# Kernel tuning notes

Measured on AMD Instinct MI355X. Metric: run time of the kernel, lower is better.

## Reference

```python
import jax, jax.numpy as jnp
import numpy as np

HE, WE, L = 361, 720, 37   # ERA5 source grid (0.5 deg) and pressure levels
HM, WM, K = 180, 360, 32   # model grid (1 deg) and model sigma levels
EPS = 1e-8

# ERA5 standard 37 pressure levels in Pa (ascending)
P_LEVELS = [100., 200., 300., 500., 700., 1000., 2000., 3000., 5000., 7000.,
            10000., 12500., 15000., 17500., 20000., 22500., 25000., 30000.,
            35000., 40000., 45000., 50000., 55000., 60000., 65000., 70000.,
            75000., 77500., 80000., 82500., 85000., 87500., 90000., 92500.,
            95000., 97500., 100000.]


def setup_inputs() -> dict:
    key = jax.random.key(0)
    ks = jax.random.split(key, 6)
    u = 10.0 * jax.random.normal(ks[0], (HE, WE, L), jnp.float32)
    v = 10.0 * jax.random.normal(ks[1], (HE, WE, L), jnp.float32)
    w = 0.1 * jax.random.normal(ks[2], (HE, WE, L), jnp.float32)
    T = 250.0 + 30.0 * jax.random.normal(ks[3], (HE, WE, L), jnp.float32)
    q = 0.01 * jax.random.uniform(ks[4], (HE, WE, L), jnp.float32)
    ps = 95000.0 + 5000.0 * jax.random.normal(ks[5], (HE, WE), jnp.float32)
    era5_lat = jnp.linspace(-90.0, 90.0, HE, dtype=jnp.float32)
    era5_lon = jnp.linspace(0.0, 359.5, WE, dtype=jnp.float32)
    model_lat = jnp.linspace(-89.0, 89.0, HM, dtype=jnp.float32)
    model_lon = jnp.linspace(0.25, 359.75, WM, dtype=jnp.float32)
    p_levels = jnp.asarray(P_LEVELS, jnp.float32)
    b_k = ((jnp.arange(K, dtype=jnp.float32) + 0.5) / K)
    a_k = 100.0 * (1.0 - b_k)  # simple hybrid coefficients (Pa)
    return dict(u=u, v=v, w=w, T=T, q=q, ps=ps,
                era5_lat=era5_lat, era5_lon=era5_lon,
                model_lat=model_lat, model_lon=model_lon,
                p_levels=p_levels, a_k=a_k, b_k=b_k)


def _axis_interp(grid, pts):
    """1D linear interp indices/weights with linear extrapolation (fill_value=None)."""
    i = jnp.clip(jnp.searchsorted(grid, pts, side='right') - 1, 0, grid.shape[0] - 2)
    t = (pts - grid[i]) / (grid[i + 1] - grid[i])
    return i, t


def _forward(u, v, w, T, q, ps, era5_lat, era5_lon, model_lat, model_lon,
             p_levels, a_k, b_k):
    # ---- horizontal bilinear interp (RegularGridInterpolator, linear) ----
    stacked = jnp.concatenate([u, v, w, T, q, ps[..., None]], axis=-1)  # [HE,WE,5L+1]
    iy, ty = _axis_interp(era5_lat, model_lat)   # [HM]
    ix, tx = _axis_interp(era5_lon, model_lon)   # [WM]
    r0 = stacked[iy]       # [HM,WE,C]
    r1 = stacked[iy + 1]
    d00, d01 = r0[:, ix], r0[:, ix + 1]          # [HM,WM,C]
    d10, d11 = r1[:, ix], r1[:, ix + 1]
    wy = ty[:, None, None]
    wx = tx[None, :, None]
    hd = (1 - wy) * ((1 - wx) * d00 + wx * d01) + wy * ((1 - wx) * d10 + wx * d11)
    vars_h = hd[..., :5 * L].reshape(HM, WM, 5, L)  # [HM,WM,5,L]
    ps_m = hd[..., -1]                               # [HM,WM]

    # ---- model pressure: p = a_k + b_k * ps ----
    p_model = a_k + b_k * ps_m[..., None]            # [HM,WM,K]

    # ---- vertical log-pressure linear interp with per-pixel valid mask ----
    logp_e = jnp.log(p_levels + EPS)                 # [L]
    logp_m = jnp.log(p_model + EPS)                  # [HM,WM,K]
    nvalid = jnp.searchsorted(p_levels, ps_m, side='right')  # levels with p<=ps
    idx = jnp.searchsorted(logp_e, logp_m, side='right') - 1
    idx = jnp.clip(idx, 0, jnp.maximum(nvalid[..., None] - 2, 0))  # [HM,WM,K]
    x0, x1 = logp_e[idx], logp_e[idx + 1]
    t = (logp_m - x0) / (x1 - x0)                    # linear extrapolation at edges
    g0 = jnp.take_along_axis(vars_h, idx[:, :, None, :], axis=3)        # [HM,WM,5,K]
    g1 = jnp.take_along_axis(vars_h, (idx + 1)[:, :, None, :], axis=3)
    out = g0 + t[:, :, None, :] * (g1 - g0)
    out = jnp.where(nvalid[:, :, None, None] >= 2, out, 0.0)            # <2 valid -> 0

    # ---- unit conversion / clamps ----
    u_o, v_o, w_o = out[:, :, 0], out[:, :, 1], out[:, :, 2]
    T_o = jnp.clip(out[:, :, 3], 150.0, 350.0)
    q_o = jnp.clip(out[:, :, 4], 0.0, 0.05)
    ps_o = jnp.clip(ps_m, 30000.0, 110000.0)
    out3d = jnp.stack([u_o, v_o, w_o, T_o, q_o], axis=-1)  # [HM,WM,K,5]
    return out3d, p_model, ps_o


def reference(u, v, w, T, q, ps, era5_lat, era5_lon, model_lat, model_lon,
              p_levels, a_k, b_k):
    return _forward(u, v, w, T, q, ps, era5_lat, era5_lon,
                    model_lat, model_lon, p_levels, a_k, b_k)
```

## Files before the change

kernel.cpp:

```cpp
#include <hip/hip_runtime.h>
#include <cmath>

#define HE 361
#define WE 720
#define LL 37
#define HM 180
#define WM 360
#define KK 32
#define NPTS (HM * WM)
#define EPSF 1e-8f
#define PTSB 8

#define OFF1 ((size_t)HM * WM * KK * 5)
#define OFF2 (OFF1 + (size_t)HM * WM * KK)

#define WS_IY    0
#define WS_TY    180
#define WS_IX    360
#define WS_TX    720
#define WS_LOGPE 1080

__device__ __forceinline__ int upper_bound_g(const float* a, int n, float v) {
    int lo = 0, hi = n;
    while (lo < hi) {
        int m = (lo + hi) >> 1;
        if (a[m] <= v) lo = m + 1; else hi = m;
    }
    return lo;
}

__global__ void precompute_kernel(const float* __restrict__ era5_lat,
                                  const float* __restrict__ era5_lon,
                                  const float* __restrict__ model_lat,
                                  const float* __restrict__ model_lon,
                                  const float* __restrict__ p_levels,
                                  int* __restrict__ ws_iy, float* __restrict__ ws_ty,
                                  int* __restrict__ ws_ix, float* __restrict__ ws_tx,
                                  float* __restrict__ ws_logpe) {
    int t = blockIdx.x * blockDim.x + threadIdx.x;
    if (t < HM) {
        float v = model_lat[t];
        int i = upper_bound_g(era5_lat, HE, v) - 1;
        if (i < 0) i = 0;
        if (i > HE - 2) i = HE - 2;
        ws_iy[t] = i;
        ws_ty[t] = (v - era5_lat[i]) / (era5_lat[i + 1] - era5_lat[i]);
    } else if (t < HM + WM) {
        int j = t - HM;
        float v = model_lon[j];
        int i = upper_bound_g(era5_lon, WE, v) - 1;
        if (i < 0) i = 0;
        if (i > WE - 2) i = WE - 2;
        ws_ix[j] = i;
        ws_tx[j] = (v - era5_lon[i]) / (era5_lon[i + 1] - era5_lon[i]);
    } else if (t < HM + WM + LL) {
        int k = t - HM - WM;
        ws_logpe[k] = logf(p_levels[k] + EPSF);
    }
}

__global__ void __launch_bounds__(256)
fused_kernel(const float* __restrict__ u, const float* __restrict__ v,
             const float* __restrict__ w, const float* __restrict__ T,
             const float* __restrict__ q, const float* __restrict__ ps,
             const float* __restrict__ p_levels,
             const float* __restrict__ a_k, const float* __restrict__ b_k,
             const int* __restrict__ ws_iy, const float* __restrict__ ws_ty,
             const int* __restrict__ ws_ix, const float* __restrict__ ws_tx,
             const float* __restrict__ ws_logpe,
             float* __restrict__ out) {
    __shared__ float s_h[PTSB][5 * LL];
    __shared__ float s_psm[PTSB];
    __shared__ float s_plev[LL];
    __shared__ float s_logpe[LL];
    __shared__ float s_ak[KK];
    __shared__ float s_bk[KK];

    const int tid = threadIdx.x;
    if (tid < LL) {
        s_plev[tid]  = p_levels[tid];
        s_logpe[tid] = ws_logpe[tid];
    } else if (tid >= 64 && tid < 64 + KK) {
        s_ak[tid - 64] = a_k[tid - 64];
        s_bk[tid - 64] = b_k[tid - 64];
    }

    const int pt_local = tid >> 5;
    const int grp      = tid & 31;
    const int pt = blockIdx.x * PTSB + pt_local;
    const int y  = pt / WM;
    const int x  = pt - y * WM;

    const int   iy = ws_iy[y];
    const float ty = ws_ty[y];
    const int   ix = ws_ix[x];
    const float tx = ws_tx[x];
    const float omty = 1.0f - ty;
    const float omtx = 1.0f - tx;

    const size_t b00 = (size_t)iy * WE + ix;

    if (grp == 0) {
        const float p00 = ps[b00], p01 = ps[b00 + 1];
        const float p10 = ps[b00 + WE], p11 = ps[b00 + WE + 1];
        const float ps_m = omty * (omtx * p00 + tx * p01) + ty * (omtx * p10 + tx * p11);
        s_psm[pt_local] = ps_m;
        out[OFF2 + pt] = fminf(fmaxf(ps_m, 30000.0f), 110000.0f);
    }

    const float* srcs0 = u;
    const float* srcs1 = v;
    const float* srcs2 = w;
    const float* srcs3 = T;
    const float* srcs4 = q;

#pragma unroll
    for (int it = 0; it < 6; it++) {
        const int ch = grp + 32 * it;
        if (ch < 5 * LL) {
            const int var = ch / LL;
            const int l   = ch - var * LL;
            const float* s = (var == 0) ? srcs0 : (var == 1) ? srcs1
                           : (var == 2) ? srcs2 : (var == 3) ? srcs3 : srcs4;
            const size_t c00 = b00 * LL + l;
            const float d00 = s[c00];
            const float d01 = s[c00 + LL];
            const float d10 = s[c00 + (size_t)WE * LL];
            const float d11 = s[c00 + (size_t)WE * LL + LL];
            s_h[pt_local][ch] = omty * (omtx * d00 + tx * d01) +
                                ty   * (omtx * d10 + tx * d11);
        }
    }

    __syncthreads();

    const int k = grp;
    const float ps_m = s_psm[pt_local];

    int nvalid = 0;
#pragma unroll
    for (int l = 0; l < LL; l++) nvalid += (s_plev[l] <= ps_m) ? 1 : 0;
    int maxi = nvalid - 2;
    if (maxi < 0) maxi = 0;

    const float pm = s_ak[k] + s_bk[k] * ps_m;
    out[OFF1 + (size_t)pt * KK + k] = pm;

    const float lpm = logf(pm + EPSF);
    int lo = 0, hi = LL;
    while (lo < hi) {
        int m = (lo + hi) >> 1;
        if (s_logpe[m] <= lpm) lo = m + 1; else hi = m;
    }
    int i = lo - 1;
    if (i < 0) i = 0;
    if (i > maxi) i = maxi;
    const float t = (lpm - s_logpe[i]) / (s_logpe[i + 1] - s_logpe[i]);

    const bool invalid = (nvalid < 2);
    const size_t obase = (size_t)pt * (KK * 5) + k * 5;
#pragma unroll
    for (int var = 0; var < 5; var++) {
        const float g0 = s_h[pt_local][var * LL + i];
        const float g1 = s_h[pt_local][var * LL + i + 1];
        float o = g0 + t * (g1 - g0);
        if (invalid) o = 0.0f;
        if (var == 3) o = fminf(fmaxf(o, 150.0f), 350.0f);
        if (var == 4) o = fminf(fmaxf(o, 0.0f), 0.05f);
        out[obase + var] = o;
    }
}

extern "C" void kernel_launch(void* const* d_in, const int* in_sizes, int n_in,
                              void* d_out, int out_size, void* d_ws, size_t ws_size,
                              hipStream_t stream) {
    const float* u         = (const float*)d_in[0];
    const float* v         = (const float*)d_in[1];
    const float* w         = (const float*)d_in[2];
    const float* T         = (const float*)d_in[3];
    const float* q         = (const float*)d_in[4];
    const float* ps        = (const float*)d_in[5];
    const float* era5_lat  = (const float*)d_in[6];
    const float* era5_lon  = (const float*)d_in[7];
    const float* model_lat = (const float*)d_in[8];
    const float* model_lon = (const float*)d_in[9];
    const float* p_levels  = (const float*)d_in[10];
    const float* a_k       = (const float*)d_in[11];
    const float* b_k       = (const float*)d_in[12];

    float* wsf = (float*)d_ws;
    int*   ws_iy    = (int*)(wsf + WS_IY);
    float* ws_ty    = wsf + WS_TY;
    int*   ws_ix    = (int*)(wsf + WS_IX);
    float* ws_tx    = wsf + WS_TX;
    float* ws_logpe = wsf + WS_LOGPE;

    float* out = (float*)d_out;

    precompute_kernel<<<3, 256, 0, stream>>>(era5_lat, era5_lon, model_lat, model_lon,
                                             p_levels, ws_iy, ws_ty, ws_ix, ws_tx,
                                             ws_logpe);

    const int blocks = NPTS / PTSB;
    fused_kernel<<<blocks, 256, 0, stream>>>(u, v, w, T, q, ps, p_levels, a_k, b_k,
                                             ws_iy, ws_ty, ws_ix, ws_tx, ws_logpe, out);
}
```

Baseline: 231.0 us.

## Stage shared source columns into LDS via global_load_lds and defer horizontal interp

Each block now stages a 2-row by 9-column patch of all five source variables (all 37 levels) into LDS using the asynchronous global_load_lds path, instead of having each point gather its own 4 corners. Horizontal bilinear interpolation is deferred and done per output level only for the two bracketing pressure levels, reading corners from LDS. Adjacent model points share source columns, so the change aims to remove redundant global gathers and register staging. It keeps a global-memory fallback for points whose columns fall outside the staged patch. The cost is a larger LDS footprint and more corner reads per output level, which may reduce occupancy.

```diff
diff --git a/kernel.cpp b/kernel.cpp
--- a/kernel.cpp
+++ b/kernel.cpp
@@ -1,5 +1,6 @@
 #include <hip/hip_runtime.h>
 #include <cmath>
+#include <stdint.h>
 
 #define HE 361
 #define WE 720
@@ -10,6 +11,11 @@
 #define NPTS (HM * WM)
 #define EPSF 1e-8f
 #define PTSB 8
+#define NC 9
+#define NSEG (2 * NC * 5)
+#define TOTF (NSEG * LL)
+#define NIT ((TOTF + 255) / 256)
+#define LDSF (NIT * 256)
 
 #define OFF1 ((size_t)HM * WM * KK * 5)
 #define OFF2 (OFF1 + (size_t)HM * WM * KK)
@@ -69,7 +75,7 @@
              const int* __restrict__ ws_ix, const float* __restrict__ ws_tx,
              const float* __restrict__ ws_logpe,
              float* __restrict__ out) {
-    __shared__ float s_h[PTSB][5 * LL];
+    __shared__ float s_cols[LDSF];
     __shared__ float s_psm[PTSB];
     __shared__ float s_plev[LL];
     __shared__ float s_logpe[LL];
@@ -77,6 +83,35 @@
     __shared__ float s_bk[KK];
 
     const int tid = threadIdx.x;
+    const int pt0 = blockIdx.x * PTSB;
+    const int y   = pt0 / WM;
+    const int x0  = pt0 - y * WM;
+
+    const int   iy    = ws_iy[y];
+    const int   colLo = ws_ix[x0];
+
+    const int wavebase = __builtin_amdgcn_readfirstlane(tid & ~63);
+#pragma unroll
+    for (int it = 0; it < NIT; it++) {
+        int idx = it * 256 + tid;
+        int idc = (idx < TOTF) ? idx : (TOTF - 1);
+        int seg = idc / LL;
+        int l   = idc - seg * LL;
+        int r   = seg / (NC * 5);
+        int rem = seg - r * (NC * 5);
+        int c   = rem / 5;
+        int var = rem - c * 5;
+        int col = colLo + c;
+        if (col > WE - 1) col = WE - 1;
+        const float* sp = (var == 0) ? u : (var == 1) ? v : (var == 2) ? w
+                        : (var == 3) ? T : q;
+        const float* ga = sp + ((size_t)(iy + r) * WE + col) * LL + l;
+        __builtin_amdgcn_global_load_lds(
+            (const __attribute__((address_space(1))) uint32_t*)ga,
+            (__attribute__((address_space(3))) uint32_t*)&s_cols[it * 256 + wavebase],
+            4, 0, 0);
+    }
+
     if (tid < LL) {
         s_plev[tid]  = p_levels[tid];
         s_logpe[tid] = ws_logpe[tid];
@@ -87,20 +122,17 @@
 
     const int pt_local = tid >> 5;
     const int grp      = tid & 31;
-    const int pt = blockIdx.x * PTSB + pt_local;
-    const int y  = pt / WM;
-    const int x  = pt - y * WM;
-
-    const int   iy = ws_iy[y];
+    const int pt = pt0 + pt_local;
+    const int x  = x0 + pt_local;
+
     const float ty = ws_ty[y];
-    const int   ix = ws_ix[x];
     const float tx = ws_tx[x];
+    const int   ixp = ws_ix[x];
     const float omty = 1.0f - ty;
     const float omtx = 1.0f - tx;
 
-    const size_t b00 = (size_t)iy * WE + ix;
-
     if (grp == 0) {
+        const size_t b00 = (size_t)iy * WE + ixp;
         const float p00 = ps[b00], p01 = ps[b00 + 1];
         const float p10 = ps[b00 + WE], p11 = ps[b00 + WE + 1];
         const float ps_m = omty * (omtx * p00 + tx * p01) + ty * (omtx * p10 + tx * p11);
@@ -108,30 +140,6 @@
         out[OFF2 + pt] = fminf(fmaxf(ps_m, 30000.0f), 110000.0f);
     }
 
-    const float* srcs0 = u;
-    const float* srcs1 = v;
-    const float* srcs2 = w;
-    const float* srcs3 = T;
-    const float* srcs4 = q;
-
-#pragma unroll
-    for (int it = 0; it < 6; it++) {
-        const int ch = grp + 32 * it;
-        if (ch < 5 * LL) {
-            const int var = ch / LL;
-            const int l   = ch - var * LL;
-            const float* s = (var == 0) ? srcs0 : (var == 1) ? srcs1
-                           : (var == 2) ? srcs2 : (var == 3) ? srcs3 : srcs4;
-            const size_t c00 = b00 * LL + l;
-            const float d00 = s[c00];
-            const float d01 = s[c00 + LL];
-            const float d10 = s[c00 + (size_t)WE * LL];
-            const float d11 = s[c00 + (size_t)WE * LL + LL];
-            s_h[pt_local][ch] = omty * (omtx * d00 + tx * d01) +
-                                ty   * (omtx * d10 + tx * d11);
-        }
-    }
-
     __syncthreads();
 
     const int k = grp;
@@ -159,15 +167,49 @@
 
     const bool invalid = (nvalid < 2);
     const size_t obase = (size_t)pt * (KK * 5) + k * 5;
-#pragma unroll
-    for (int var = 0; var < 5; var++) {
-        const float g0 = s_h[pt_local][var * LL + i];
-        const float g1 = s_h[pt_local][var * LL + i + 1];
-        float o = g0 + t * (g1 - g0);
-        if (invalid) o = 0.0f;
-        if (var == 3) o = fminf(fmaxf(o, 150.0f), 350.0f);
-        if (var == 4) o = fminf(fmaxf(o, 0.0f), 0.05f);
-        out[obase + var] = o;
+
+    const int cpt = ixp - colLo;
+    if (cpt >= 0 && cpt <= NC - 2) {
+        const int o00 = (cpt * 5) * LL;
+        const int o01 = ((cpt + 1) * 5) * LL;
+        const int o10 = ((NC + cpt) * 5) * LL;
+        const int o11 = ((NC + cpt + 1) * 5) * LL;
+#pragma unroll
+        for (int var = 0; var < 5; var++) {
+            const int vb = var * LL + i;
+            const float a0 = s_cols[o00 + vb],     b0 = s_cols[o01 + vb];
+            const float c0 = s_cols[o10 + vb],     d0 = s_cols[o11 + vb];
+            const float a1 = s_cols[o00 + vb + 1], b1 = s_cols[o01 + vb + 1];
+            const float c1 = s_cols[o10 + vb + 1], d1 = s_cols[o11 + vb + 1];
+            const float g0 = omty * (omtx * a0 + tx * b0) + ty * (omtx * c0 + tx * d0);
+            const float g1 = omty * (omtx * a1 + tx * b1) + ty * (omtx * c1 + tx * d1);
+            float o = g0 + t * (g1 - g0);
+            if (invalid) o = 0.0f;
+            if (var == 3) o = fminf(fmaxf(o, 150.0f), 350.0f);
+            if (var == 4) o = fminf(fmaxf(o, 0.0f), 0.05f);
+            out[obase + var] = o;
+        }
+    } else {
+        const size_t c00 = ((size_t)iy * WE + ixp) * LL;
+        const size_t c01 = c00 + LL;
+        const size_t c10 = c00 + (size_t)WE * LL;
+        const size_t c11 = c10 + LL;
+#pragma unroll
+        for (int var = 0; var < 5; var++) {
+            const float* sp = (var == 0) ? u : (var == 1) ? v : (var == 2) ? w
+                            : (var == 3) ? T : q;
+            const float a0 = sp[c00 + i], b0 = sp[c01 + i];
+            const float c0 = sp[c10 + i], d0 = sp[c11 + i];
+            const float a1 = sp[c00 + i + 1], b1 = sp[c01 + i + 1];
+            const float c1 = sp[c10 + i + 1], d1 = sp[c11 + i + 1];
+            const float g0 = omty * (omtx * a0 + tx * b0) + ty * (omtx * c0 + tx * d0);
+            const float g1 = omty * (omtx * a1 + tx * b1) + ty * (omtx * c1 + tx * d1);
+            float o = g0 + t * (g1 - g0);
+            if (invalid) o = 0.0f;
+            if (var == 3) o = fminf(fmaxf(o, 150.0f), 350.0f);
+            if (var == 4) o = fminf(fmaxf(o, 0.0f), 0.05f);
+            out[obase + var] = o;
+        }
     }
 }
 
```

Measured after the change: 236.1 us. 1.02x slower.
